# Performance work log

Hardware: AMD Instinct MI355X
Metric: run time of the kernel (lower is better)

Reference implementation:

```python
import jax, jax.numpy as jnp
import numpy as np
import math

B, N, D_IN, D_OUT, H = 8, 1024, 512, 512, 8
DH = D_OUT // H  # 64
SCALE = math.sqrt(DH)

def setup_inputs() -> dict:
    key = jax.random.key(0)
    ks = jax.random.split(key, 10)
    s_in = 1.0 / math.sqrt(D_IN)
    s_out = 1.0 / math.sqrt(D_OUT)
    return {
        "x": jax.random.normal(ks[0], (B, N, D_IN), dtype=jnp.float32),
        "Wq": jax.random.uniform(ks[1], (D_IN, D_OUT), jnp.float32, -s_in, s_in),
        "bq": jnp.zeros((D_OUT,), jnp.float32),
        "Wk": jax.random.uniform(ks[2], (D_IN, D_OUT), jnp.float32, -s_in, s_in),
        "bk": jnp.zeros((D_OUT,), jnp.float32),
        "Wv": jax.random.uniform(ks[3], (D_IN, D_OUT), jnp.float32, -s_in, s_in),
        "bv": jnp.zeros((D_OUT,), jnp.float32),
        "Wo": jax.random.uniform(ks[4], (D_OUT, D_OUT), jnp.float32, -s_out, s_out),
        "bo": jnp.zeros((D_OUT,), jnp.float32),
        # external distance-based positional bias buffer (num_heads, N, N)
        "pos_bias": 0.01 * jax.random.normal(ks[5], (H, N, N), dtype=jnp.float32),
    }

def reference(x, Wq, bq, Wk, bk, Wv, bv, Wo, bo, pos_bias):
    Bx, Nx, _ = x.shape
    # QKV projections -> (B, H, N, DH)
    def split_heads(t):
        return t.reshape(Bx, Nx, H, DH).transpose(0, 2, 1, 3)
    q = split_heads(x @ Wq + bq)
    k = split_heads(x @ Wk + bk)
    v = split_heads(x @ Wv + bv)
    # scaled dot-product scores with additive positional bias
    scores = jnp.einsum('bhnd,bhmd->bhnm', q, k) / SCALE + pos_bias[None]
    attn = jax.nn.softmax(scores, axis=-1)  # dropout p=0 (eval)
    out = jnp.einsum('bhnm,bhmd->bhnd', attn, v)
    out = out.transpose(0, 2, 1, 3).reshape(Bx, Nx, D_OUT)  # concat heads
    return out @ Wo + bo
```

## Files before the change

kernel.cpp:

```cpp
#include <hip/hip_runtime.h>
#include <hip/hip_bf16.h>
#include <stdint.h>


typedef __attribute__((ext_vector_type(4))) float f32x4;
typedef __attribute__((ext_vector_type(8))) short s16x8;
typedef __attribute__((ext_vector_type(4))) unsigned short u16x4;
typedef __attribute__((ext_vector_type(8))) unsigned short u16x8;

union FragAB { s16x8 v; u16x4 h[2]; unsigned u[4]; };

#define LOG2E 1.44269504089f
#define QSCALE (0.125f * LOG2E)

__device__ __forceinline__ unsigned short f2b(float f) {
  unsigned u = __builtin_bit_cast(unsigned, f);
  u = (u + 0x7FFFu + ((u >> 16) & 1u)) >> 16;
  return (unsigned short)u;
}
__device__ __forceinline__ unsigned pack2f(float lo, float hi) {
  const unsigned short a = __builtin_bit_cast(unsigned short, __float2bfloat16(lo));
  const unsigned short b = __builtin_bit_cast(unsigned short, __float2bfloat16(hi));
  return ((unsigned)b << 16) | (unsigned)a;
}

__global__ __launch_bounds__(256) void prep_k(const float* __restrict__ x,
                                              unsigned short* __restrict__ xb,
                                              const float* __restrict__ W0,
                                              const float* __restrict__ W1,
                                              const float* __restrict__ W2,
                                              const float* __restrict__ W3,
                                              unsigned short* __restrict__ Wt) {
  __shared__ float ld[64][68];
  const int t = threadIdx.x;
  if (blockIdx.x < 4096) {
    int idx = blockIdx.x * 256 + t;
    f32x4 v = ((const f32x4*)x)[idx];
    u16x4 o;
#pragma unroll
    for (int j = 0; j < 4; j++) o[j] = f2b(v[j]);
    ((u16x4*)xb)[idx] = o;
    return;
  }
  const int bid2 = blockIdx.x - 4096;
  const int widx = bid2 >> 6;
  const int tile = bid2 & 63;
  const int trow = tile >> 3, tcol = tile & 7;
  const float* W = widx == 0 ? W0 : widx == 1 ? W1 : widx == 2 ? W2 : W3;
  const int r = t >> 2, cc = (t & 3) * 16;
  const float* src = W + (size_t)(trow * 64 + r) * 512 + tcol * 64 + cc;
#pragma unroll
  for (int u = 0; u < 4; u++)
    ((f32x4*)&ld[r][cc])[u] = ((const f32x4*)src)[u];
  __syncthreads();
  unsigned short* dst = Wt + ((size_t)widx << 18) + (size_t)(tcol * 64 + r) * 512 +
                        trow * 64 + cc;
#pragma unroll
  for (int u = 0; u < 4; u++) {
    u16x4 o;
#pragma unroll
    for (int e = 0; e < 4; e++) o[e] = f2b(ld[cc + u * 4 + e][r]);
    ((u16x4*)dst)[u] = o;
  }
}

__global__ __launch_bounds__(256, 2) void gemm_qkv_k(const unsigned short* __restrict__ A,
                                                     const unsigned short* __restrict__ Bt,
                                                     const float* __restrict__ bq,
                                                     const float* __restrict__ bk,
                                                     const float* __restrict__ bv,
                                                     unsigned short* __restrict__ outp) {
  __shared__ unsigned short At[2][128][36];
  __shared__ unsigned short Bts[2][128][36];
  const int tid = threadIdx.x;
  const int lane = tid & 63;
  const int w = tid >> 6;
  const int wm = w >> 1, wn = w & 1;
  const int g = lane >> 4, c = lane & 15;
  const int bn0 = (blockIdx.x % 12) * 128;
  const int bm0 = (blockIdx.x / 12) * 128;
  const int srow = tid >> 1;
  const int scol = (tid & 1) * 16;

  f32x4 acc[4][4];
#pragma unroll
  for (int i = 0; i < 4; i++)
#pragma unroll
    for (int j = 0; j < 4; j++) acc[i][j] = f32x4{0.f, 0.f, 0.f, 0.f};

  u16x4 ra[4], rb[4];
  auto ld = [&](int kt) {
    const u16x4* pa = (const u16x4*)(A + (size_t)(bm0 + srow) * 512 + kt * 32 + scol);
    const u16x4* pb = (const u16x4*)(Bt + (size_t)(bn0 + srow) * 512 + kt * 32 + scol);
#pragma unroll
    for (int j = 0; j < 4; j++) { ra[j] = pa[j]; rb[j] = pb[j]; }
  };
  auto st = [&](int b) {
    u16x4* da = (u16x4*)&At[b][srow][scol];
    u16x4* db = (u16x4*)&Bts[b][srow][scol];
#pragma unroll
    for (int j = 0; j < 4; j++) { da[j] = ra[j]; db[j] = rb[j]; }
  };

  ld(0); st(0);
  __syncthreads();

  for (int kt = 0; kt < 16; ++kt) {
    const int cb = kt & 1;
    if (kt < 15) ld(kt + 1);

    FragAB af[4], bf[4];
#pragma unroll
    for (int mi = 0; mi < 4; mi++) {
      const u16x4* p = (const u16x4*)&At[cb][wm * 64 + mi * 16 + c][g * 8];
      af[mi].h[0] = p[0]; af[mi].h[1] = p[1];
    }
#pragma unroll
    for (int ni = 0; ni < 4; ni++) {
      const u16x4* p = (const u16x4*)&Bts[cb][wn * 64 + ni * 16 + c][g * 8];
      bf[ni].h[0] = p[0]; bf[ni].h[1] = p[1];
    }
    __builtin_amdgcn_s_setprio(1);
#pragma unroll
    for (int mi = 0; mi < 4; mi++)
#pragma unroll
      for (int ni = 0; ni < 4; ni++)
        acc[mi][ni] = __builtin_amdgcn_mfma_f32_16x16x32_bf16(af[mi].v, bf[ni].v,
                                                              acc[mi][ni], 0, 0, 0);
    __builtin_amdgcn_s_setprio(0);

    if (kt < 15) {
      st(cb ^ 1);
      __syncthreads();
    }
  }

  const int qkv = (bn0 + wn * 64) >> 9;
  const float* bp = qkv == 0 ? bq : (qkv == 1 ? bk : bv);
  const float scale = qkv == 0 ? QSCALE : 1.0f;
#pragma unroll
  for (int mi = 0; mi < 4; mi++) {
#pragma unroll
    for (int ni = 0; ni < 4; ni++) {
      const int col = bn0 + wn * 64 + ni * 16 + c;
      const int c9 = col & 511;
      const float bvv = bp[c9];
#pragma unroll
      for (int m = 0; m < 4; m++) {
        const int row = bm0 + wm * 64 + mi * 16 + g * 4 + m;
        const float v = (acc[mi][ni][m] + bvv) * scale;
        const int b = row >> 10, n = row & 1023;
        const int hh = c9 >> 6, d = col & 63;
        if (qkv == 2) {
          outp[((size_t)2 << 22) + ((size_t)((b << 3) + hh) << 16) +
               ((size_t)d << 10) + n] = f2b(v);
        } else {
          outp[((size_t)qkv << 22) + ((size_t)((b << 3) + hh) << 16) +
               ((size_t)n << 6) + d] = f2b(v);
        }
      }
    }
  }
}

__global__ __launch_bounds__(512, 2) void gemm_o_k(const unsigned short* __restrict__ A,
                                                   const unsigned short* __restrict__ Bt,
                                                   const float* __restrict__ bias,
                                                   float* __restrict__ outp) {
  __shared__ unsigned short At[2][128][36];
  __shared__ unsigned short Bts[2][128][36];
  const int tid = threadIdx.x;
  const int lane = tid & 63;
  const int w = tid >> 6;
  const int wm = w >> 1, wn = w & 1;
  const int g = lane >> 4, c = lane & 15;
  const int bn0 = (blockIdx.x & 3) * 128;
  const int bm0 = (blockIdx.x >> 2) * 128;
  const int srow = tid >> 2;
  const int scol = (tid & 3) * 8;

  f32x4 acc[2][4];
#pragma unroll
  for (int i = 0; i < 2; i++)
#pragma unroll
    for (int j = 0; j < 4; j++) acc[i][j] = f32x4{0.f, 0.f, 0.f, 0.f};

  u16x8 ra, rb;
  auto ld = [&](int kt) {
    ra = *(const u16x8*)(A + (size_t)(bm0 + srow) * 512 + kt * 32 + scol);
    rb = *(const u16x8*)(Bt + (size_t)(bn0 + srow) * 512 + kt * 32 + scol);
  };
  auto st = [&](int b) {
    *(u16x8*)&At[b][srow][scol] = ra;
    *(u16x8*)&Bts[b][srow][scol] = rb;
  };

  ld(0); st(0);
  __syncthreads();

  for (int kt = 0; kt < 16; ++kt) {
    const int cb = kt & 1;
    if (kt < 15) ld(kt + 1);

    FragAB af[2], bf[4];
#pragma unroll
    for (int mi = 0; mi < 2; mi++) {
      const u16x4* p = (const u16x4*)&At[cb][wm * 32 + mi * 16 + c][g * 8];
      af[mi].h[0] = p[0]; af[mi].h[1] = p[1];
    }
#pragma unroll
    for (int ni = 0; ni < 4; ni++) {
      const u16x4* p = (const u16x4*)&Bts[cb][wn * 64 + ni * 16 + c][g * 8];
      bf[ni].h[0] = p[0]; bf[ni].h[1] = p[1];
    }
    __builtin_amdgcn_s_setprio(1);
#pragma unroll
    for (int mi = 0; mi < 2; mi++)
#pragma unroll
      for (int ni = 0; ni < 4; ni++)
        acc[mi][ni] = __builtin_amdgcn_mfma_f32_16x16x32_bf16(af[mi].v, bf[ni].v,
                                                              acc[mi][ni], 0, 0, 0);
    __builtin_amdgcn_s_setprio(0);

    if (kt < 15) {
      st(cb ^ 1);
      __syncthreads();
    }
  }

#pragma unroll
  for (int mi = 0; mi < 2; mi++) {
#pragma unroll
    for (int ni = 0; ni < 4; ni++) {
      const int col = bn0 + wn * 64 + ni * 16 + c;
      const float bv = bias[col];
#pragma unroll
      for (int m = 0; m < 4; m++) {
        const int row = bm0 + wm * 32 + mi * 16 + g * 4 + m;
        outp[(size_t)row * 512 + col] = acc[mi][ni][m] + bv;
      }
    }
  }
}

__global__ __launch_bounds__(256, 2) void attn_k(const unsigned short* __restrict__ Qb,
                                                 const unsigned short* __restrict__ Kb,
                                                 const unsigned short* __restrict__ Vt,
                                                 const float* __restrict__ pos_bias,
                                                 unsigned short* __restrict__ ao) {
  __shared__ unsigned short Klds[2][64][68];
  __shared__ unsigned short Vtlds[2][64][68];
  __shared__ unsigned short Plds[4][32][68];

  const int tid = threadIdx.x;
  const int lane = tid & 63;
  const int w = tid >> 6;
  const int g = lane >> 4, c = lane & 15;
  const int L = blockIdx.x;
  const int qt = L >> 6;
  const int bh = (L & 7) + 8 * ((L >> 3) & 7);
  const int h = bh & 7;
  const size_t bhq = (size_t)bh << 16;
  const int q0 = qt * 128 + w * 32;

  FragAB aq[2][2];
#pragma unroll
  for (int mi = 0; mi < 2; mi++)
#pragma unroll
    for (int kk = 0; kk < 2; kk++) {
      const u16x4* p = (const u16x4*)(Qb + bhq + ((size_t)(q0 + mi * 16 + c) << 6) +
                                      kk * 32 + g * 8);
      aq[mi][kk].h[0] = p[0]; aq[mi][kk].h[1] = p[1];
    }

  f32x4 acco[2][4];
#pragma unroll
  for (int mi = 0; mi < 2; mi++)
#pragma unroll
    for (int nd = 0; nd < 4; nd++) acco[mi][nd] = f32x4{0.f, 0.f, 0.f, 0.f};
  float lsum[2] = {0.f, 0.f};

  const int srow = tid >> 2;
  const int scol = (tid & 3) * 16;
  const unsigned short* pK = Kb + bhq + ((size_t)srow << 6) + scol;
  const unsigned short* pV = Vt + bhq + ((size_t)srow << 10) + scol;

  u16x8 kr0, kr1, vr0, vr1;
  auto stageLoad = [&](int k0n) {
    const u16x8* a = (const u16x8*)(pK + ((size_t)k0n << 6));
    kr0 = a[0]; kr1 = a[1];
    const u16x8* b = (const u16x8*)(pV + k0n);
    vr0 = b[0]; vr1 = b[1];
  };
  auto stageWrite = [&](int b) {
    *(u16x8*)&Klds[b][srow][scol] = kr0;
    *(u16x8*)&Klds[b][srow][scol + 8] = kr1;
    *(u16x8*)&Vtlds[b][srow][scol] = vr0;
    *(u16x8*)&Vtlds[b][srow][scol + 8] = vr1;
  };

  const float* pbB = pos_bias + ((size_t)h << 20) + ((size_t)(q0 + c) << 10) + 4 * g;

  stageLoad(0);
  stageWrite(0);
  __syncthreads();

  for (int kt = 0; kt < 16; ++kt) {
    const int buf = kt & 1;
    const int k0 = kt << 6;
    if (kt < 15) stageLoad(k0 + 64);

    f32x4 pb[2][4];
#pragma unroll
    for (int mi = 0; mi < 2; mi++)
#pragma unroll
      for (int ni = 0; ni < 4; ni++)
        pb[mi][ni] = *(const f32x4*)(pbB + (mi << 14) + k0 + 16 * ni);

    FragAB bk[4][2];
#pragma unroll
    for (int ni = 0; ni < 4; ni++)
#pragma unroll
      for (int kk = 0; kk < 2; kk++) {
        const u16x4* p = (const u16x4*)&Klds[buf][ni * 16 + c][kk * 32 + g * 8];
        bk[ni][kk].h[0] = p[0]; bk[ni][kk].h[1] = p[1];
      }
    f32x4 sT[2][4];
    __builtin_amdgcn_s_setprio(1);
#pragma unroll
    for (int mi = 0; mi < 2; mi++)
#pragma unroll
      for (int ni = 0; ni < 4; ni++) {
        f32x4 s = f32x4{0.f, 0.f, 0.f, 0.f};
        s = __builtin_amdgcn_mfma_f32_16x16x32_bf16(bk[ni][0].v, aq[mi][0].v, s, 0, 0, 0);
        s = __builtin_amdgcn_mfma_f32_16x16x32_bf16(bk[ni][1].v, aq[mi][1].v, s, 0, 0, 0);
        sT[mi][ni] = s;
      }
    __builtin_amdgcn_s_setprio(0);

#pragma unroll
    for (int mi = 0; mi < 2; mi++)
#pragma unroll
      for (int ni = 0; ni < 4; ni++) {
        const float p0 = __builtin_amdgcn_exp2f(fmaf(pb[mi][ni][0], LOG2E, sT[mi][ni][0]));
        const float p1 = __builtin_amdgcn_exp2f(fmaf(pb[mi][ni][1], LOG2E, sT[mi][ni][1]));
        const float p2 = __builtin_amdgcn_exp2f(fmaf(pb[mi][ni][2], LOG2E, sT[mi][ni][2]));
        const float p3 = __builtin_amdgcn_exp2f(fmaf(pb[mi][ni][3], LOG2E, sT[mi][ni][3]));
        lsum[mi] += (p0 + p1) + (p2 + p3);
        uint2 two;
        two.x = pack2f(p0, p1);
        two.y = pack2f(p2, p3);
        *(uint2*)&Plds[w][mi * 16 + c][16 * ni + 4 * g] = two;
      }

    asm volatile("s_waitcnt lgkmcnt(0)" ::: "memory");

    FragAB paf[2][2], vb2[4][2];
#pragma unroll
    for (int mi = 0; mi < 2; mi++)
#pragma unroll
      for (int kc = 0; kc < 2; kc++) {
        const u16x4* p = (const u16x4*)&Plds[w][mi * 16 + c][kc * 32 + g * 8];
        paf[mi][kc].h[0] = p[0]; paf[mi][kc].h[1] = p[1];
      }
#pragma unroll
    for (int nd = 0; nd < 4; nd++)
#pragma unroll
      for (int kc = 0; kc < 2; kc++) {
        const u16x4* p = (const u16x4*)&Vtlds[buf][nd * 16 + c][kc * 32 + g * 8];
        vb2[nd][kc].h[0] = p[0]; vb2[nd][kc].h[1] = p[1];
      }
    __builtin_amdgcn_s_setprio(1);
#pragma unroll
    for (int mi = 0; mi < 2; mi++)
#pragma unroll
      for (int nd = 0; nd < 4; nd++) {
        acco[mi][nd] = __builtin_amdgcn_mfma_f32_16x16x32_bf16(paf[mi][0].v, vb2[nd][0].v,
                                                               acco[mi][nd], 0, 0, 0);
        acco[mi][nd] = __builtin_amdgcn_mfma_f32_16x16x32_bf16(paf[mi][1].v, vb2[nd][1].v,
                                                               acco[mi][nd], 0, 0, 0);
      }
    __builtin_amdgcn_s_setprio(0);

    if (kt < 15) {
      stageWrite(buf ^ 1);
      __syncthreads();
    }
  }

  const int b = bh >> 3;
#pragma unroll
  for (int mi = 0; mi < 2; mi++) {
    float l = lsum[mi];
    l += __shfl_xor(l, 16);
    l += __shfl_xor(l, 32);
    const float inv_c = 1.f / l;
#pragma unroll
    for (int m = 0; m < 4; m++) {
      const float invm = __shfl(inv_c, g * 4 + m);
      const int n = q0 + mi * 16 + g * 4 + m;
#pragma unroll
      for (int nd = 0; nd < 4; nd++) {
        ao[((size_t)(b * 1024 + n) << 9) + h * 64 + nd * 16 + c] =
            f2b(acco[mi][nd][m] * invm);
      }
    }
  }
}

extern "C" void kernel_launch(void* const* d_in, const int* in_sizes, int n_in,
                              void* d_out, int out_size, void* d_ws, size_t ws_size,
                              hipStream_t stream) {
  (void)in_sizes; (void)n_in; (void)out_size; (void)ws_size;
  const float* x  = (const float*)d_in[0];
  const float* Wq = (const float*)d_in[1];
  const float* bq = (const float*)d_in[2];
  const float* Wk = (const float*)d_in[3];
  const float* bk = (const float*)d_in[4];
  const float* Wv = (const float*)d_in[5];
  const float* bv = (const float*)d_in[6];
  const float* Wo = (const float*)d_in[7];
  const float* bo = (const float*)d_in[8];
  const float* pbias = (const float*)d_in[9];

  char* p = (char*)d_ws;
  unsigned short* xb  = (unsigned short*)p; p += (size_t)8192 * 512 * 2;
  unsigned short* WT  = (unsigned short*)p; p += (size_t)4 * 512 * 512 * 2;
  unsigned short* Qb  = (unsigned short*)p; p += (size_t)3 * 64 * 1024 * 64 * 2;
  unsigned short* AO  = (unsigned short*)p;

  unsigned short* WoT = WT + (size_t)3 * 512 * 512;
  unsigned short* Kb  = Qb + (size_t)64 * 1024 * 64;
  unsigned short* Vb  = Kb + (size_t)64 * 1024 * 64;

  prep_k<<<4352, 256, 0, stream>>>(x, xb, Wq, Wk, Wv, Wo, WT);
  gemm_qkv_k<<<768, 256, 0, stream>>>(xb, WT, bq, bk, bv, Qb);
  attn_k<<<512, 256, 0, stream>>>(Qb, Kb, Vb, pbias, AO);
  gemm_o_k<<<256, 512, 0, stream>>>(AO, WoT, bo, (float*)d_out);
}
```

Measured before the change: 88.84 us.

## Use direct global-to-LDS loads in QKV GEMM, LDS-transposed V store, packed bf16 cvt

The QKV GEMM now stages A and B tiles with global_load_lds straight into unpadded shared memory, skipping the register round trip. The V-output epilogue transposes through LDS so stores are coalesced along n instead of scattered 2-byte writes. Attention swaps software bf16 packing for the v_cvt_pk_bf16_f32 instruction and hoists the V fragment loads above the exp computation. Removing the LDS padding may add bank conflicts on fragment reads, and the wait on vmcnt(0) before each barrier limits overlap of loads with compute.

```diff
diff --git a/kernel.cpp b/kernel.cpp
--- a/kernel.cpp
+++ b/kernel.cpp
@@ -18,10 +18,15 @@
   u = (u + 0x7FFFu + ((u >> 16) & 1u)) >> 16;
   return (unsigned short)u;
 }
-__device__ __forceinline__ unsigned pack2f(float lo, float hi) {
-  const unsigned short a = __builtin_bit_cast(unsigned short, __float2bfloat16(lo));
-  const unsigned short b = __builtin_bit_cast(unsigned short, __float2bfloat16(hi));
-  return ((unsigned)b << 16) | (unsigned)a;
+__device__ __forceinline__ unsigned cvt_pk(float a, float b) {
+  unsigned r;
+  asm("v_cvt_pk_bf16_f32 %0, %1, %2" : "=v"(r) : "v"(a), "v"(b));
+  return r;
+}
+__device__ __forceinline__ void gl_lds16(const unsigned short* g, unsigned short* l) {
+  __builtin_amdgcn_global_load_lds(
+      (const __attribute__((address_space(1))) unsigned int*)(g),
+      (__attribute__((address_space(3))) unsigned int*)(l), 16, 0, 0);
 }
 
 __global__ __launch_bounds__(256) void prep_k(const float* __restrict__ x,
@@ -70,8 +75,7 @@
                                                      const float* __restrict__ bk,
                                                      const float* __restrict__ bv,
                                                      unsigned short* __restrict__ outp) {
-  __shared__ unsigned short At[2][128][36];
-  __shared__ unsigned short Bts[2][128][36];
+  __shared__ unsigned short SM[2][2][128][32];
   const int tid = threadIdx.x;
   const int lane = tid & 63;
   const int w = tid >> 6;
@@ -79,8 +83,6 @@
   const int g = lane >> 4, c = lane & 15;
   const int bn0 = (blockIdx.x % 12) * 128;
   const int bm0 = (blockIdx.x / 12) * 128;
-  const int srow = tid >> 1;
-  const int scol = (tid & 1) * 16;
 
   f32x4 acc[4][4];
 #pragma unroll
@@ -88,36 +90,36 @@
 #pragma unroll
     for (int j = 0; j < 4; j++) acc[i][j] = f32x4{0.f, 0.f, 0.f, 0.f};
 
-  u16x4 ra[4], rb[4];
-  auto ld = [&](int kt) {
-    const u16x4* pa = (const u16x4*)(A + (size_t)(bm0 + srow) * 512 + kt * 32 + scol);
-    const u16x4* pb = (const u16x4*)(Bt + (size_t)(bn0 + srow) * 512 + kt * 32 + scol);
-#pragma unroll
-    for (int j = 0; j < 4; j++) { ra[j] = pa[j]; rb[j] = pb[j]; }
+  auto stage = [&](int buf, int kt) {
+#pragma unroll
+    for (int j = 0; j < 2; j++) {
+      const int qb = (j * 4 + w) * 64;
+      const int chunk = qb + lane;
+      const int row = chunk >> 2, slot = chunk & 3;
+      gl_lds16(A + (size_t)(bm0 + row) * 512 + kt * 32 + slot * 8,
+               &SM[buf][0][0][0] + qb * 8);
+      gl_lds16(Bt + (size_t)(bn0 + row) * 512 + kt * 32 + slot * 8,
+               &SM[buf][1][0][0] + qb * 8);
+    }
   };
-  auto st = [&](int b) {
-    u16x4* da = (u16x4*)&At[b][srow][scol];
-    u16x4* db = (u16x4*)&Bts[b][srow][scol];
-#pragma unroll
-    for (int j = 0; j < 4; j++) { da[j] = ra[j]; db[j] = rb[j]; }
-  };
-
-  ld(0); st(0);
+
+  stage(0, 0);
+  asm volatile("s_waitcnt vmcnt(0)" ::: "memory");
   __syncthreads();
 
   for (int kt = 0; kt < 16; ++kt) {
     const int cb = kt & 1;
-    if (kt < 15) ld(kt + 1);
+    if (kt < 15) stage(cb ^ 1, kt + 1);
 
     FragAB af[4], bf[4];
 #pragma unroll
     for (int mi = 0; mi < 4; mi++) {
-      const u16x4* p = (const u16x4*)&At[cb][wm * 64 + mi * 16 + c][g * 8];
+      const u16x4* p = (const u16x4*)&SM[cb][0][wm * 64 + mi * 16 + c][g * 8];
       af[mi].h[0] = p[0]; af[mi].h[1] = p[1];
     }
 #pragma unroll
     for (int ni = 0; ni < 4; ni++) {
-      const u16x4* p = (const u16x4*)&Bts[cb][wn * 64 + ni * 16 + c][g * 8];
+      const u16x4* p = (const u16x4*)&SM[cb][1][wn * 64 + ni * 16 + c][g * 8];
       bf[ni].h[0] = p[0]; bf[ni].h[1] = p[1];
     }
     __builtin_amdgcn_s_setprio(1);
@@ -130,36 +132,64 @@
     __builtin_amdgcn_s_setprio(0);
 
     if (kt < 15) {
-      st(cb ^ 1);
+      asm volatile("s_waitcnt vmcnt(0)" ::: "memory");
       __syncthreads();
     }
   }
+
+  __syncthreads();
 
   const int qkv = (bn0 + wn * 64) >> 9;
   const float* bp = qkv == 0 ? bq : (qkv == 1 ? bk : bv);
   const float scale = qkv == 0 ? QSCALE : 1.0f;
-#pragma unroll
-  for (int mi = 0; mi < 4; mi++) {
-#pragma unroll
-    for (int ni = 0; ni < 4; ni++) {
-      const int col = bn0 + wn * 64 + ni * 16 + c;
-      const int c9 = col & 511;
-      const float bvv = bp[c9];
-#pragma unroll
-      for (int m = 0; m < 4; m++) {
-        const int row = bm0 + wm * 64 + mi * 16 + g * 4 + m;
-        const float v = (acc[mi][ni][m] + bvv) * scale;
-        const int b = row >> 10, n = row & 1023;
-        const int hh = c9 >> 6, d = col & 63;
-        if (qkv == 2) {
-          outp[((size_t)2 << 22) + ((size_t)((b << 3) + hh) << 16) +
-               ((size_t)d << 10) + n] = f2b(v);
-        } else {
+  const int b = (bm0 + wm * 64) >> 10;
+  const int nb = (bm0 + wm * 64) & 1023;
+
+  if (qkv == 2) {
+    unsigned short* T = &SM[0][0][0][0] + w * 2176;
+    const int hh = ((bn0 + wn * 64) & 511) >> 6;
+    unsigned short* dst = outp + ((size_t)2 << 22) + ((size_t)((b << 3) + hh) << 16) + nb;
+#pragma unroll
+    for (int r2 = 0; r2 < 2; r2++) {
+#pragma unroll
+      for (int ni2 = 0; ni2 < 2; ni2++) {
+        const int ni = r2 * 2 + ni2;
+        const int dloc = ni2 * 16 + c;
+        const float bvv = bp[(bn0 + wn * 64 + ni * 16 + c) & 511];
+#pragma unroll
+        for (int mi = 0; mi < 4; mi++) {
+          const int n = mi * 16 + g * 4;
+          *(unsigned*)&T[dloc * 68 + n] =
+              cvt_pk(acc[mi][ni][0] + bvv, acc[mi][ni][1] + bvv);
+          *(unsigned*)&T[dloc * 68 + n + 2] =
+              cvt_pk(acc[mi][ni][2] + bvv, acc[mi][ni][3] + bvv);
+        }
+      }
+      asm volatile("s_waitcnt lgkmcnt(0)" ::: "memory");
+#pragma unroll
+      for (int r = 0; r < 8; r++) {
+        const int dloc = r * 4 + g;
+        const u16x4 v4 = *(const u16x4*)&T[dloc * 68 + c * 4];
+        *(u16x4*)(dst + ((size_t)(r2 * 32 + dloc) << 10) + c * 4) = v4;
+      }
+      if (r2 == 0) asm volatile("s_waitcnt lgkmcnt(0)" ::: "memory");
+    }
+  } else {
+#pragma unroll
+    for (int mi = 0; mi < 4; mi++)
+#pragma unroll
+      for (int ni = 0; ni < 4; ni++) {
+        const int c9 = (bn0 + wn * 64 + ni * 16 + c) & 511;
+        const float bvv = bp[c9];
+        const int hh = c9 >> 6, d = c9 & 63;
+#pragma unroll
+        for (int m = 0; m < 4; m++) {
+          const int n = nb + mi * 16 + g * 4 + m;
+          const float v = (acc[mi][ni][m] + bvv) * scale;
           outp[((size_t)qkv << 22) + ((size_t)((b << 3) + hh) << 16) +
                ((size_t)n << 6) + d] = f2b(v);
         }
       }
-    }
   }
 }
 
@@ -289,8 +319,8 @@
   auto stageLoad = [&](int k0n) {
     const u16x8* a = (const u16x8*)(pK + ((size_t)k0n << 6));
     kr0 = a[0]; kr1 = a[1];
-    const u16x8* b = (const u16x8*)(pV + k0n);
-    vr0 = b[0]; vr1 = b[1];
+    const u16x8* bb = (const u16x8*)(pV + k0n);
+    vr0 = bb[0]; vr1 = bb[1];
   };
   auto stageWrite = [&](int b) {
     *(u16x8*)&Klds[b][srow][scol] = kr0;
@@ -338,6 +368,15 @@
       }
     __builtin_amdgcn_s_setprio(0);
 
+    FragAB vb2[4][2];
+#pragma unroll
+    for (int nd = 0; nd < 4; nd++)
+#pragma unroll
+      for (int kc = 0; kc < 2; kc++) {
+        const u16x4* p = (const u16x4*)&Vtlds[buf][nd * 16 + c][kc * 32 + g * 8];
+        vb2[nd][kc].h[0] = p[0]; vb2[nd][kc].h[1] = p[1];
+      }
+
 #pragma unroll
     for (int mi = 0; mi < 2; mi++)
 #pragma unroll
@@ -348,27 +387,20 @@
         const float p3 = __builtin_amdgcn_exp2f(fmaf(pb[mi][ni][3], LOG2E, sT[mi][ni][3]));
         lsum[mi] += (p0 + p1) + (p2 + p3);
         uint2 two;
-        two.x = pack2f(p0, p1);
-        two.y = pack2f(p2, p3);
+        two.x = cvt_pk(p0, p1);
+        two.y = cvt_pk(p2, p3);
         *(uint2*)&Plds[w][mi * 16 + c][16 * ni + 4 * g] = two;
       }
 
     asm volatile("s_waitcnt lgkmcnt(0)" ::: "memory");
 
-    FragAB paf[2][2], vb2[4][2];
+    FragAB paf[2][2];
 #pragma unroll
     for (int mi = 0; mi < 2; mi++)
 #pragma unroll
       for (int kc = 0; kc < 2; kc++) {
         const u16x4* p = (const u16x4*)&Plds[w][mi * 16 + c][kc * 32 + g * 8];
         paf[mi][kc].h[0] = p[0]; paf[mi][kc].h[1] = p[1];
-      }
-#pragma unroll
-    for (int nd = 0; nd < 4; nd++)
-#pragma unroll
-      for (int kc = 0; kc < 2; kc++) {
-        const u16x4* p = (const u16x4*)&Vtlds[buf][nd * 16 + c][kc * 32 + g * 8];
-        vb2[nd][kc].h[0] = p[0]; vb2[nd][kc].h[1] = p[1];
       }
     __builtin_amdgcn_s_setprio(1);
 #pragma unroll
```

Measured after the change: 81.60 us. 1.09x faster.
